# Performance work log

Hardware: AMD Instinct MI355X
Metric: run time of the kernel (lower is better)

The kernel has to match this reference:

```python
import jax, jax.numpy as jnp
import numpy as np

N, D_IN, D_HID, D_OUT = 100000, 128, 512, 256
EPS = 1e-5


def _kaiming_uniform(k, shape):
    # torch kaiming_uniform_(a=sqrt(5)) -> bound = sqrt(1/fan_in)
    fan_in = shape[1]
    bound = float(np.sqrt(1.0 / fan_in))
    return jax.random.uniform(k, shape, minval=-bound, maxval=bound, dtype=jnp.float32)


def setup_inputs() -> dict:
    key = jax.random.key(0)
    ks = jax.random.split(key, 10)
    in_set = jax.random.normal(ks[0], (N, D_IN), dtype=jnp.float32)
    matA0 = _kaiming_uniform(ks[1], (D_HID, D_IN))
    matB0 = _kaiming_uniform(ks[2], (D_HID, D_IN))
    matA1 = _kaiming_uniform(ks[3], (D_HID, D_HID))
    matB1 = _kaiming_uniform(ks[4], (D_HID, D_HID))
    matA2 = _kaiming_uniform(ks[5], (D_HID, D_HID))
    matB2 = _kaiming_uniform(ks[6], (D_HID, D_HID))
    ln_gamma = jnp.ones((D_HID,), dtype=jnp.float32)
    ln_beta = jnp.zeros((D_HID,), dtype=jnp.float32)
    out_bound = float(np.sqrt(1.0 / D_HID))
    out_w = jax.random.uniform(ks[7], (D_OUT, D_HID), minval=-out_bound, maxval=out_bound, dtype=jnp.float32)
    out_b = jax.random.uniform(ks[8], (D_OUT,), minval=-out_bound, maxval=out_bound, dtype=jnp.float32)
    return {"in_set": in_set, "matA0": matA0, "matB0": matB0, "matA1": matA1, "matB1": matB1,
            "matA2": matA2, "matB2": matB2, "ln_gamma": ln_gamma, "ln_beta": ln_beta,
            "out_w": out_w, "out_b": out_b}


def _layer(h, A, B, g, b):
    # f(x_i) = relu(LN(A x_i + B (sum_j x_j - x_i)))
    # vectorized: h @ (A-B)^T + total_sum @ B^T  (sum-minus-self identity)
    s = h.sum(axis=0)  # [d]
    h = h @ (A - B).T + s @ B.T  # [N, d_hid]
    mu = h.mean(axis=-1, keepdims=True)
    var = jnp.mean((h - mu) ** 2, axis=-1, keepdims=True)
    h = (h - mu) / jnp.sqrt(var + EPS) * g + b
    return jax.nn.relu(h)


def reference(in_set, matA0, matB0, matA1, matB1, matA2, matB2, ln_gamma, ln_beta, out_w, out_b):
    h = _layer(in_set, matA0, matB0, ln_gamma, ln_beta)
    h = _layer(h, matA1, matB1, ln_gamma, ln_beta)
    h = _layer(h, matA2, matB2, ln_gamma, ln_beta)
    h = h.max(axis=0)  # max-pool over set elements -> [d_hid]
    return h @ out_w.T + out_b  # [d_out]
```

## Files before the change

### kernel.cpp

```cpp
#include <hip/hip_runtime.h>
#include <hip/hip_bf16.h>

#define NPTS 100000
#define NPTS_PAD 100096
#define DHID 512
#define EPSV 1e-5f

typedef __attribute__((ext_vector_type(4))) float f32x4;

#define OFF_INBF   0UL
#define OFF_W0     12812288UL
#define OFF_W1     12877824UL
#define OFF_W2     13139968UL
#define OFF_C0     13402112UL
#define OFF_C1     13404160UL
#define OFF_C2     13406208UL
#define OFF_PARTS  13408256UL
#define OFF_PARTS2 16609280UL
#define OFF_PARTS3 16740352UL
#define OFF_H1     16756736UL
#define OFF_H2     68005888UL

typedef const __attribute__((address_space(1))) unsigned int* gp_t;
typedef __attribute__((address_space(3))) unsigned int* lp_t;

__device__ __forceinline__ void async_copy16(const void* g, void* l) {
    __builtin_amdgcn_global_load_lds((gp_t)g, (lp_t)l, 16, 0, 0);
}

__device__ __forceinline__ unsigned pack4_fp8(float a, float b, float c, float d) {
    unsigned v = (unsigned)__builtin_amdgcn_cvt_pk_fp8_f32(a, b, 0, false);
    v = (unsigned)__builtin_amdgcn_cvt_pk_fp8_f32(c, d, (int)v, true);
    return v;
}

__global__ __launch_bounds__(256) void cvt_pack_kernel(const float* __restrict__ in,
                                                       unsigned char* __restrict__ out) {
    long total = (long)NPTS * 2;
    long stride = (long)gridDim.x * blockDim.x;
    for (long idx = (long)blockIdx.x * blockDim.x + threadIdx.x; idx < total; idx += stride) {
        int kt = (int)(idx / NPTS);
        long r = idx - (long)kt * NPTS;
        const float* src = in + r * 128 + kt * 64;
        unsigned dw[16];
#pragma unroll
        for (int m = 0; m < 16; ++m)
            dw[m] = pack4_fp8(src[m], src[16 + m], src[32 + m], src[48 + m]);
        uint4* dst = (uint4*)(out + ((long)kt * NPTS_PAD + r) * 64);
#pragma unroll
        for (int j = 0; j < 4; ++j)
            dst[j] = make_uint4(dw[4 * j], dw[4 * j + 1], dw[4 * j + 2], dw[4 * j + 3]);
    }
}

__global__ __launch_bounds__(256) void wpack_all_kernel(const float* __restrict__ A0,
                                                        const float* __restrict__ B0,
                                                        const float* __restrict__ A1,
                                                        const float* __restrict__ B1,
                                                        const float* __restrict__ A2,
                                                        const float* __restrict__ B2,
                                                        unsigned long long* __restrict__ W0,
                                                        unsigned long long* __restrict__ W1,
                                                        unsigned long long* __restrict__ W2) {
    int idx = blockIdx.x * 256 + threadIdx.x;
    const float *A, *B; unsigned long long* W; int KD, u;
    if (idx < 8192)       { A = A0; B = B0; W = W0; KD = 128; u = idx; }
    else if (idx < 40960) { A = A1; B = B1; W = W1; KD = 512; u = idx - 8192; }
    else                  { A = A2; B = B2; W = W2; KD = 512; u = idx - 40960; if (u >= 32768) return; }
    int F = (KD / 64) * 8;
    int lane = u & 63;
    int f = (u >> 6) % F;
    int wid = u / (64 * F);
    int ks = f >> 3, fn = (f >> 1) & 3, s = f & 1;
    int ln15 = lane & 15, lg = lane >> 4;
    int row = wid * 64 + fn * 16 + ln15;
    int c0 = s * 8 + lg * 2;
    const float* sa = A + (long)row * KD + ks * 64;
    const float* sb = B + (long)row * KD + ks * 64;
    unsigned lo = pack4_fp8(sa[c0] - sb[c0], sa[16 + c0] - sb[16 + c0],
                            sa[32 + c0] - sb[32 + c0], sa[48 + c0] - sb[48 + c0]);
    unsigned hi = pack4_fp8(sa[c0 + 1] - sb[c0 + 1], sa[17 + c0] - sb[17 + c0],
                            sa[33 + c0] - sb[33 + c0], sa[49 + c0] - sb[49 + c0]);
    W[u] = ((unsigned long long)hi << 32) | lo;
}

__global__ __launch_bounds__(256) void colsum_in_kernel(const float* __restrict__ in,
                                                        float* __restrict__ parts) {
    __shared__ float sh[256];
    int t = threadIdx.x, blk = blockIdx.x;
    int c = t & 127, half = t >> 7;
    long rbeg = (long)blk * 196 + half;
    long rend = (long)(blk + 1) * 196; if (rend > NPTS) rend = NPTS;
    float s = 0.f;
    for (long r = rbeg; r < rend; r += 2) s += in[r * 128 + c];
    sh[t] = s;
    __syncthreads();
    if (t < 128) parts[blk * 128 + t] = sh[t] + sh[t + 128];
}

__global__ void part_reduceW_kernel(const float* __restrict__ parts, int nparts, int width,
                                    int op, float* __restrict__ out) {
    int g = blockIdx.x, t = threadIdx.x;
    int chunk = (nparts + gridDim.x - 1) / gridDim.x;
    int b0 = g * chunk, b1 = b0 + chunk; if (b1 > nparts) b1 = nparts;
    float s = 0.f;
    for (int b = b0; b < b1; ++b) {
        float v = parts[(long)b * width + t];
        s = (op == 0) ? (s + v) : fmaxf(s, v);
    }
    out[(long)g * width + t] = s;
}

__global__ __launch_bounds__(64) void gemv_fold_kernel(const float* __restrict__ p3, int dsum,
                                                       const float* __restrict__ Bm,
                                                       const float* __restrict__ bias, int op,
                                                       float* __restrict__ out) {
    int j = blockIdx.x, t = threadIdx.x;
    float acc = 0.f;
    for (int d = t; d < dsum; d += 64) {
        float s = 0.f;
#pragma unroll
        for (int g = 0; g < 8; ++g) {
            float v = p3[(long)g * dsum + d];
            s = (op == 0) ? (s + v) : fmaxf(s, v);
        }
        acc += s * Bm[(long)j * dsum + d];
    }
#pragma unroll
    for (int m = 32; m >= 1; m >>= 1) acc += __shfl_down(acc, m);
    if (t == 0) out[j] = acc + (bias ? bias[j] : 0.0f);
}

template<int KD, bool STORE, int REDOP>
__global__ __launch_bounds__(512, 4)
void layer_kernel(const unsigned char* __restrict__ Xp, const unsigned long long* __restrict__ Wp,
                  const float* __restrict__ cvec, const float* __restrict__ gvec,
                  const float* __restrict__ bvec, unsigned char* __restrict__ Hout,
                  float* __restrict__ red_out) {
    static_assert(KD % 64 == 0, "");
    constexpr int NK = KD / 64;
    __shared__ __align__(128) char smem[NK * 4096];

    const int t = threadIdx.x;
    const int lane = t & 63;
    const int wid = t >> 6;
    const int ln15 = lane & 15;
    const int lg = lane >> 4;
    const long row0 = (long)blockIdx.x * 64;

    f32x4 acc[4][4];
#pragma unroll
    for (int i = 0; i < 4; ++i)
#pragma unroll
        for (int j = 0; j < 4; ++j) acc[i][j] = (f32x4){0.f, 0.f, 0.f, 0.f};

    if (t < 256) {
        const int sr = t >> 2;
        const int ss = t & 3;
        const char* Xsrc = (const char*)Xp + (row0 + sr) * 64 + ((ss ^ ((sr >> 1) & 3)) * 16);
#pragma unroll
        for (int kt = 0; kt < NK; ++kt)
            async_copy16(Xsrc + (long)kt * (NPTS_PAD * 64), smem + kt * 4096 + t * 16);
    }
    __syncthreads();

#define RD8X(BASE, r, sub) (*(const long*)((BASE) + (r) * 64 + \
        (((((sub) * 2 + (lg >> 1)) ^ (((r) >> 1) & 3)) * 16) + (lg & 1) * 8)))

    const unsigned long long* Wq = Wp + (long)wid * (NK * 8) * 64 + lane;
#pragma unroll
    for (int ks = 0; ks < NK; ++ks) {
        const char* Xs = smem + ks * 4096;
        long a0[4], a1[4];
#pragma unroll
        for (int fm = 0; fm < 4; ++fm) {
            int r = fm * 16 + ln15;
            a0[fm] = RD8X(Xs, r, 0);
            a1[fm] = RD8X(Xs, r, 1);
        }
#pragma unroll
        for (int fn = 0; fn < 4; ++fn) {
            long w0 = (long)Wq[(ks * 8 + fn * 2 + 0) * 64];
            long w1 = (long)Wq[(ks * 8 + fn * 2 + 1) * 64];
#pragma unroll
            for (int fm = 0; fm < 4; ++fm)
                acc[fm][fn] = __builtin_amdgcn_mfma_f32_16x16x32_fp8_fp8(a0[fm], w0, acc[fm][fn], 0, 0, 0);
#pragma unroll
            for (int fm = 0; fm < 4; ++fm)
                acc[fm][fn] = __builtin_amdgcn_mfma_f32_16x16x32_fp8_fp8(a1[fm], w1, acc[fm][fn], 0, 0, 0);
        }
    }
#undef RD8X
    __syncthreads();

    float* lnred_s = (float*)smem;
    float* lnred_q = (float*)(smem + 2048);
    float* lnmv    = (float*)(smem + 4096);

    const int cbase = wid * 64 + ln15;
    float cv[4], gv[4], bv[4];
#pragma unroll
    for (int fn = 0; fn < 4; ++fn) {
        int col = cbase + fn * 16;
        cv[fn] = cvec[col]; gv[fn] = gvec[col]; bv[fn] = bvec[col];
    }

#pragma unroll
    for (int fm = 0; fm < 4; ++fm)
#pragma unroll
        for (int fn = 0; fn < 4; ++fn) acc[fm][fn] += cv[fn];

    float rs[16], rq[16];
#pragma unroll
    for (int fm = 0; fm < 4; ++fm)
#pragma unroll
        for (int j = 0; j < 4; ++j) {
            float s = 0.f, q = 0.f;
#pragma unroll
            for (int fn = 0; fn < 4; ++fn) {
                float x = acc[fm][fn][j];
                s += x; q += x * x;
            }
            rs[fm * 4 + j] = s; rq[fm * 4 + j] = q;
        }
#pragma unroll
    for (int m = 1; m < 16; m <<= 1)
#pragma unroll
        for (int i = 0; i < 16; ++i) {
            rs[i] += __shfl_xor(rs[i], m);
            rq[i] += __shfl_xor(rq[i], m);
        }
    if (ln15 == 0) {
#pragma unroll
        for (int fm = 0; fm < 4; ++fm)
#pragma unroll
            for (int j = 0; j < 4; ++j) {
                int row = fm * 16 + lg * 4 + j;
                lnred_s[row * 8 + wid] = rs[fm * 4 + j];
                lnred_q[row * 8 + wid] = rq[fm * 4 + j];
            }
    }
    __syncthreads();
    if (t < 64) {
        float s = 0.f, q = 0.f;
#pragma unroll
        for (int w = 0; w < 8; ++w) { s += lnred_s[t * 8 + w]; q += lnred_q[t * 8 + w]; }
        float mu = s * (1.0f / 512.0f);
        float var = q * (1.0f / 512.0f) - mu * mu;
        lnmv[t * 2] = mu;
        lnmv[t * 2 + 1] = rsqrtf(var + EPSV);
    }
    __syncthreads();

#pragma unroll
    for (int fm = 0; fm < 4; ++fm)
#pragma unroll
        for (int j = 0; j < 4; ++j) {
            int rloc = fm * 16 + lg * 4 + j;
            long rglob = row0 + rloc;
            bool ok = rglob < NPTS;
            float mu = lnmv[rloc * 2], rstd = lnmv[rloc * 2 + 1];
#pragma unroll
            for (int fn = 0; fn < 4; ++fn) {
                float y = fmaxf((acc[fm][fn][j] - mu) * rstd * gv[fn] + bv[fn], 0.0f);
                acc[fm][fn][j] = ok ? y : 0.0f;
            }
            if (STORE) {
                unsigned u = pack4_fp8(acc[fm][0][j], acc[fm][1][j], acc[fm][2][j], acc[fm][3][j]);
                *(unsigned*)(Hout + ((long)wid * NPTS_PAD + rglob) * 64 + ln15 * 4) = u;
            }
        }

    float cp[4];
#pragma unroll
    for (int fn = 0; fn < 4; ++fn) {
        float p = 0.f;
#pragma unroll
        for (int fm = 0; fm < 4; ++fm)
#pragma unroll
            for (int j = 0; j < 4; ++j) {
                float v = acc[fm][fn][j];
                p = (REDOP == 0) ? (p + v) : fmaxf(p, v);
            }
        cp[fn] = p;
    }
#pragma unroll
    for (int m = 16; m < 64; m <<= 1)
#pragma unroll
        for (int fn = 0; fn < 4; ++fn) {
            float o = __shfl_xor(cp[fn], m);
            cp[fn] = (REDOP == 0) ? (cp[fn] + o) : fmaxf(cp[fn], o);
        }
    if (lane < 16) {
#pragma unroll
        for (int fn = 0; fn < 4; ++fn)
            red_out[(long)blockIdx.x * 512 + wid * 64 + fn * 16 + lane] = cp[fn];
    }
}

extern "C" void kernel_launch(void* const* d_in, const int* in_sizes, int n_in,
                              void* d_out, int out_size, void* d_ws, size_t ws_size,
                              hipStream_t stream) {
    const float* in_set = (const float*)d_in[0];
    const float* A0 = (const float*)d_in[1];
    const float* B0 = (const float*)d_in[2];
    const float* A1 = (const float*)d_in[3];
    const float* B1 = (const float*)d_in[4];
    const float* A2 = (const float*)d_in[5];
    const float* B2 = (const float*)d_in[6];
    const float* ga = (const float*)d_in[7];
    const float* be = (const float*)d_in[8];
    const float* ow = (const float*)d_in[9];
    const float* ob = (const float*)d_in[10];
    float* outp = (float*)d_out;
    char* ws = (char*)d_ws;

    unsigned char* in_f8 = (unsigned char*)(ws + OFF_INBF);
    unsigned long long* W0p = (unsigned long long*)(ws + OFF_W0);
    unsigned long long* W1p = (unsigned long long*)(ws + OFF_W1);
    unsigned long long* W2p = (unsigned long long*)(ws + OFF_W2);
    float* c0 = (float*)(ws + OFF_C0);
    float* c1 = (float*)(ws + OFF_C1);
    float* c2 = (float*)(ws + OFF_C2);
    float* parts = (float*)(ws + OFF_PARTS);
    float* parts2 = (float*)(ws + OFF_PARTS2);
    float* parts3 = (float*)(ws + OFF_PARTS3);
    unsigned char* h1 = (unsigned char*)(ws + OFF_H1);
    unsigned char* h2 = (unsigned char*)(ws + OFF_H2);

    const int nblk = (NPTS + 63) / 64;

    cvt_pack_kernel<<<1024, 256, 0, stream>>>(in_set, in_f8);
    wpack_all_kernel<<<288, 256, 0, stream>>>(A0, B0, A1, B1, A2, B2, W0p, W1p, W2p);

    colsum_in_kernel<<<512, 256, 0, stream>>>(in_set, parts);
    part_reduceW_kernel<<<64, 128, 0, stream>>>(parts, 512, 128, 0, parts2);
    part_reduceW_kernel<<<8, 128, 0, stream>>>(parts2, 64, 128, 0, parts3);
    gemv_fold_kernel<<<512, 64, 0, stream>>>(parts3, 128, B0, nullptr, 0, c0);

    layer_kernel<128, true, 0><<<nblk, 512, 0, stream>>>(in_f8, W0p, c0, ga, be, h1, parts);
    part_reduceW_kernel<<<64, 512, 0, stream>>>(parts, nblk, 512, 0, parts2);
    part_reduceW_kernel<<<8, 512, 0, stream>>>(parts2, 64, 512, 0, parts3);
    gemv_fold_kernel<<<512, 64, 0, stream>>>(parts3, 512, B1, nullptr, 0, c1);

    layer_kernel<512, true, 0><<<nblk, 512, 0, stream>>>(h1, W1p, c1, ga, be, h2, parts);
    part_reduceW_kernel<<<64, 512, 0, stream>>>(parts, nblk, 512, 0, parts2);
    part_reduceW_kernel<<<8, 512, 0, stream>>>(parts2, 64, 512, 0, parts3);
    gemv_fold_kernel<<<512, 64, 0, stream>>>(parts3, 512, B2, nullptr, 0, c2);

    layer_kernel<512, false, 1><<<nblk, 512, 0, stream>>>(h2, W2p, c2, ga, be, nullptr, parts);
    part_reduceW_kernel<<<64, 512, 0, stream>>>(parts, nblk, 512, 1, parts2);
    part_reduceW_kernel<<<8, 512, 0, stream>>>(parts2, 64, 512, 1, parts3);
    gemv_fold_kernel<<<256, 64, 0, stream>>>(parts3, 512, ow, ob, 1, outp);
}
```

Measured before the change: 297.7 us.

## Switch activations to row-major fp8, double-buffer weight loads, drop a reduce stage

Activation buffers change from k-tile-major planes to row-major layout, so each row's bytes are contiguous for both the async LDS loads and the fp8 stores. Weight fragments for the next k-step are prefetched into a register double buffer to hide global-load latency behind the MFMAs. The second partial-reduction launch is removed and the gemv folds the 64 partials directly, cutting three kernel launches. The costs are more live registers under launch_bounds(512,4), possible spills, and more redundant reads of the partials inside the gemv.

```diff
diff --git a/kernel.cpp b/kernel.cpp
--- a/kernel.cpp
+++ b/kernel.cpp
@@ -17,7 +17,6 @@
 #define OFF_C2     13406208UL
 #define OFF_PARTS  13408256UL
 #define OFF_PARTS2 16609280UL
-#define OFF_PARTS3 16740352UL
 #define OFF_H1     16756736UL
 #define OFF_H2     68005888UL
 
@@ -46,7 +45,7 @@
 #pragma unroll
         for (int m = 0; m < 16; ++m)
             dw[m] = pack4_fp8(src[m], src[16 + m], src[32 + m], src[48 + m]);
-        uint4* dst = (uint4*)(out + ((long)kt * NPTS_PAD + r) * 64);
+        uint4* dst = (uint4*)(out + r * 128 + kt * 64);
 #pragma unroll
         for (int j = 0; j < 4; ++j)
             dst[j] = make_uint4(dw[4 * j], dw[4 * j + 1], dw[4 * j + 2], dw[4 * j + 3]);
@@ -111,17 +110,16 @@
     out[(long)g * width + t] = s;
 }
 
-__global__ __launch_bounds__(64) void gemv_fold_kernel(const float* __restrict__ p3, int dsum,
-                                                       const float* __restrict__ Bm,
+__global__ __launch_bounds__(64) void gemv_fold_kernel(const float* __restrict__ p2, int nfold,
+                                                       int dsum, const float* __restrict__ Bm,
                                                        const float* __restrict__ bias, int op,
                                                        float* __restrict__ out) {
     int j = blockIdx.x, t = threadIdx.x;
     float acc = 0.f;
     for (int d = t; d < dsum; d += 64) {
         float s = 0.f;
-#pragma unroll
-        for (int g = 0; g < 8; ++g) {
-            float v = p3[(long)g * dsum + d];
+        for (int g = 0; g < nfold; ++g) {
+            float v = p2[(long)g * dsum + d];
             s = (op == 0) ? (s + v) : fmaxf(s, v);
         }
         acc += s * Bm[(long)j * dsum + d];
@@ -157,10 +155,10 @@
     if (t < 256) {
         const int sr = t >> 2;
         const int ss = t & 3;
-        const char* Xsrc = (const char*)Xp + (row0 + sr) * 64 + ((ss ^ ((sr >> 1) & 3)) * 16);
+        const char* Xsrc = (const char*)Xp + (row0 + sr) * KD + ((ss ^ ((sr >> 1) & 3)) * 16);
 #pragma unroll
         for (int kt = 0; kt < NK; ++kt)
-            async_copy16(Xsrc + (long)kt * (NPTS_PAD * 64), smem + kt * 4096 + t * 16);
+            async_copy16(Xsrc + kt * 64, smem + kt * 4096 + t * 16);
     }
     __syncthreads();
 
@@ -168,8 +166,17 @@
         (((((sub) * 2 + (lg >> 1)) ^ (((r) >> 1) & 3)) * 16) + (lg & 1) * 8)))
 
     const unsigned long long* Wq = Wp + (long)wid * (NK * 8) * 64 + lane;
+    long wbuf[2][8];
+#pragma unroll
+    for (int f = 0; f < 8; ++f) wbuf[0][f] = (long)Wq[f * 64];
+
 #pragma unroll
     for (int ks = 0; ks < NK; ++ks) {
+        if (ks + 1 < NK) {
+#pragma unroll
+            for (int f = 0; f < 8; ++f)
+                wbuf[(ks + 1) & 1][f] = (long)Wq[((ks + 1) * 8 + f) * 64];
+        }
         const char* Xs = smem + ks * 4096;
         long a0[4], a1[4];
 #pragma unroll
@@ -180,14 +187,14 @@
         }
 #pragma unroll
         for (int fn = 0; fn < 4; ++fn) {
-            long w0 = (long)Wq[(ks * 8 + fn * 2 + 0) * 64];
-            long w1 = (long)Wq[(ks * 8 + fn * 2 + 1) * 64];
 #pragma unroll
             for (int fm = 0; fm < 4; ++fm)
-                acc[fm][fn] = __builtin_amdgcn_mfma_f32_16x16x32_fp8_fp8(a0[fm], w0, acc[fm][fn], 0, 0, 0);
+                acc[fm][fn] = __builtin_amdgcn_mfma_f32_16x16x32_fp8_fp8(
+                    a0[fm], wbuf[ks & 1][fn * 2 + 0], acc[fm][fn], 0, 0, 0);
 #pragma unroll
             for (int fm = 0; fm < 4; ++fm)
-                acc[fm][fn] = __builtin_amdgcn_mfma_f32_16x16x32_fp8_fp8(a1[fm], w1, acc[fm][fn], 0, 0, 0);
+                acc[fm][fn] = __builtin_amdgcn_mfma_f32_16x16x32_fp8_fp8(
+                    a1[fm], wbuf[ks & 1][fn * 2 + 1], acc[fm][fn], 0, 0, 0);
         }
     }
 #undef RD8X
@@ -267,7 +274,7 @@
             }
             if (STORE) {
                 unsigned u = pack4_fp8(acc[fm][0][j], acc[fm][1][j], acc[fm][2][j], acc[fm][3][j]);
-                *(unsigned*)(Hout + ((long)wid * NPTS_PAD + rglob) * 64 + ln15 * 4) = u;
+                *(unsigned*)(Hout + rglob * DHID + wid * 64 + ln15 * 4) = u;
             }
         }
 
@@ -324,7 +331,6 @@
     float* c2 = (float*)(ws + OFF_C2);
     float* parts = (float*)(ws + OFF_PARTS);
     float* parts2 = (float*)(ws + OFF_PARTS2);
-    float* parts3 = (float*)(ws + OFF_PARTS3);
     unsigned char* h1 = (unsigned char*)(ws + OFF_H1);
     unsigned char* h2 = (unsigned char*)(ws + OFF_H2);
 
@@ -335,21 +341,17 @@
 
     colsum_in_kernel<<<512, 256, 0, stream>>>(in_set, parts);
     part_reduceW_kernel<<<64, 128, 0, stream>>>(parts, 512, 128, 0, parts2);
-    part_reduceW_kernel<<<8, 128, 0, stream>>>(parts2, 64, 128, 0, parts3);
-    gemv_fold_kernel<<<512, 64, 0, stream>>>(parts3, 128, B0, nullptr, 0, c0);
+    gemv_fold_kernel<<<512, 64, 0, stream>>>(parts2, 64, 128, B0, nullptr, 0, c0);
 
     layer_kernel<128, true, 0><<<nblk, 512, 0, stream>>>(in_f8, W0p, c0, ga, be, h1, parts);
     part_reduceW_kernel<<<64, 512, 0, stream>>>(parts, nblk, 512, 0, parts2);
-    part_reduceW_kernel<<<8, 512, 0, stream>>>(parts2, 64, 512, 0, parts3);
-    gemv_fold_kernel<<<512, 64, 0, stream>>>(parts3, 512, B1, nullptr, 0, c1);
+    gemv_fold_kernel<<<512, 64, 0, stream>>>(parts2, 64, 512, B1, nullptr, 0, c1);
 
     layer_kernel<512, true, 0><<<nblk, 512, 0, stream>>>(h1, W1p, c1, ga, be, h2, parts);
     part_reduceW_kernel<<<64, 512, 0, stream>>>(parts, nblk, 512, 0, parts2);
-    part_reduceW_kernel<<<8, 512, 0, stream>>>(parts2, 64, 512, 0, parts3);
-    gemv_fold_kernel<<<512, 64, 0, stream>>>(parts3, 512, B2, nullptr, 0, c2);
+    gemv_fold_kernel<<<512, 64, 0, stream>>>(parts2, 64, 512, B2, nullptr, 0, c2);
 
     layer_kernel<512, false, 1><<<nblk, 512, 0, stream>>>(h2, W2p, c2, ga, be, nullptr, parts);
     part_reduceW_kernel<<<64, 512, 0, stream>>>(parts, nblk, 512, 1, parts2);
-    part_reduceW_kernel<<<8, 512, 0, stream>>>(parts2, 64, 512, 1, parts3);
-    gemv_fold_kernel<<<256, 64, 0, stream>>>(parts3, 512, ow, ob, 1, outp);
-}
+    gemv_fold_kernel<<<256, 64, 0, stream>>>(parts2, 64, 512, ow, ob, 1, outp);
+}
```

Result: slower. 690.6 us (+131.9%).
